# Kernel optimization log

Measured on AMD Instinct MI355X. Metric: run time of the kernel, lower is better.

The kernel has to match this reference:

```python
import jax, jax.numpy as jnp
import numpy as np

N, C, K, NUM_CLASS = 400000, 128, 128, 128


def setup_inputs() -> dict:
    key = jax.random.key(0)
    k1, k2, k3 = jax.random.split(key, 3)
    outputs = jax.random.normal(k1, (N, C), dtype=jnp.float32)
    labels = jax.random.randint(k2, (N,), 0, 2 * NUM_CLASS, dtype=jnp.int64 if jax.config.read('jax_enable_x64') else jnp.int32)
    global_logit = jax.random.normal(k3, (K, C), dtype=jnp.float32)
    return {"outputs": outputs, "labels": labels, "global_logit": global_logit, "k": NUM_CLASS}


def _pairwise_dist(x, protos):
    # Euclidean distance ||proto_j - x_i|| for all (i, j) without a [N,K,C] temp.
    x2 = jnp.sum(x * x, axis=1, keepdims=True)            # [N,1]
    p2 = jnp.sum(protos * protos, axis=1)[None, :]        # [1,K]
    d2 = x2 + p2 - 2.0 * (x @ protos.T)                   # [N,K]
    return jnp.sqrt(jnp.maximum(d2, 0.0))


def reference(outputs, labels, global_logit, k):
    # Rows with labels <= k-1 keep their label; rows with labels > k-1 get the
    # nearest-prototype index. Since the concatenated (labeled + pseudo-labeled)
    # set covers every row and CE-mean is order-invariant, we compute per-row
    # effective labels and a single mean cross-entropy.
    dists = _pairwise_dist(outputs, global_logit)          # [N,K]
    min_dist_labels = jnp.argmin(dists, axis=1)            # [N]
    is_labeled = labels <= (k - 1)
    labels_eff = jnp.where(is_labeled, labels, min_dist_labels)
    logp = jax.nn.log_softmax(outputs, axis=-1)            # [N,C]
    nll = -jnp.take_along_axis(logp, labels_eff[:, None].astype(jnp.int32), axis=1)[:, 0]
    return jnp.mean(nll)
```

## Files before the change

kernel.cpp:

```cpp
#include <hip/hip_runtime.h>
#include <hip/hip_bf16.h>


#define C_DIM 128
#define TILE_ROWS 32
#define NTHREADS 256
#define XSTRIDE 136
#define GRID 2048

typedef __bf16 bf16x8 __attribute__((ext_vector_type(8)));
typedef unsigned short ushort8 __attribute__((ext_vector_type(8)));
typedef float f32x4 __attribute__((ext_vector_type(4)));

union FragU { ushort8 u; bf16x8 b; };

__device__ __forceinline__ unsigned short f2bf(float f) {
    unsigned int u = __float_as_uint(f);
    u += 0x7fffu + ((u >> 16) & 1u);
    return (unsigned short)(u >> 16);
}
__device__ __forceinline__ float bf2f(unsigned short h) {
    return __uint_as_float(((unsigned int)h) << 16);
}
__device__ __forceinline__ unsigned f2ord(float s) {
    unsigned u = __float_as_uint(s);
    return (u & 0x80000000u) ? ~u : (u | 0x80000000u);
}

extern "C" __global__ void __launch_bounds__(NTHREADS)
ploss_main(const float* __restrict__ x, const int* __restrict__ labels,
           const float* __restrict__ protos, const int* __restrict__ kptr,
           float* __restrict__ accum, int n_tiles)
{
    __shared__ __attribute__((aligned(16))) unsigned short x_lds[2][TILE_ROWS * XSTRIDE];
    __shared__ float lse_lds[2][TILE_ROWS];
    __shared__ unsigned wmin_u[4][TILE_ROWS];

    const int tid  = threadIdx.x;
    const int lane = tid & 63;
    const int wave = tid >> 6;
    const int l15  = lane & 15;
    const int quad = lane >> 4;
    const int kk   = kptr[0];

    FragU bfrag[2][4];
    float p2h[2];
#pragma unroll
    for (int nt = 0; nt < 2; ++nt) {
        const int j = wave * 32 + nt * 16 + l15;
        const float* pr = protos + j * C_DIM;
        float s = 0.f;
#pragma unroll
        for (int c = 0; c < 32; c += 4) {
            float4 v = *(const float4*)(pr + quad * 32 + c);
            s += v.x*v.x + v.y*v.y + v.z*v.z + v.w*v.w;
        }
        s += __shfl_xor(s, 16);
        s += __shfl_xor(s, 32);
        p2h[nt] = 0.5f * s;
#pragma unroll
        for (int kt = 0; kt < 4; ++kt) {
            const float* pp = pr + kt * 32 + quad * 8;
            float4 v0 = *(const float4*)(pp);
            float4 v1 = *(const float4*)(pp + 4);
            FragU f;
            f.u[0]=f2bf(v0.x); f.u[1]=f2bf(v0.y); f.u[2]=f2bf(v0.z); f.u[3]=f2bf(v0.w);
            f.u[4]=f2bf(v1.x); f.u[5]=f2bf(v1.y); f.u[6]=f2bf(v1.z); f.u[7]=f2bf(v1.w);
            bfrag[nt][kt] = f;
        }
    }

    const int row_r = tid >> 3;
    const int row_q = tid & 7;

    float nll_acc = 0.f;
    int p = 0;

    int t = blockIdx.x;
    float4 a0, a1, a2, a3;
    int lab = 0;
    {
        const float* xr = x + ((long long)t * TILE_ROWS + row_r) * C_DIM + row_q * 16;
        a0 = *(const float4*)(xr);
        a1 = *(const float4*)(xr + 4);
        a2 = *(const float4*)(xr + 8);
        a3 = *(const float4*)(xr + 12);
        if (tid < TILE_ROWS) lab = labels[(long long)t * TILE_ROWS + tid];
    }

    for (; t < n_tiles; t += GRID) {
        const int tn = t + GRID;
        const int tl = (tn < n_tiles) ? tn : t;
        float4 b0, b1, b2, b3;
        int labn = 0;
        {
            const float* xr = x + ((long long)tl * TILE_ROWS + row_r) * C_DIM + row_q * 16;
            b0 = *(const float4*)(xr);
            b1 = *(const float4*)(xr + 4);
            b2 = *(const float4*)(xr + 8);
            b3 = *(const float4*)(xr + 12);
            if (tid < TILE_ROWS) labn = labels[(long long)tl * TILE_ROWS + tid];
        }

        float m = fmaxf(fmaxf(fmaxf(a0.x,a0.y),fmaxf(a0.z,a0.w)),
                        fmaxf(fmaxf(a1.x,a1.y),fmaxf(a1.z,a1.w)));
        m = fmaxf(m, fmaxf(fmaxf(fmaxf(a2.x,a2.y),fmaxf(a2.z,a2.w)),
                           fmaxf(fmaxf(a3.x,a3.y),fmaxf(a3.z,a3.w))));
        float s = __expf(a0.x-m)+__expf(a0.y-m)+__expf(a0.z-m)+__expf(a0.w-m)
                + __expf(a1.x-m)+__expf(a1.y-m)+__expf(a1.z-m)+__expf(a1.w-m)
                + __expf(a2.x-m)+__expf(a2.y-m)+__expf(a2.z-m)+__expf(a2.w-m)
                + __expf(a3.x-m)+__expf(a3.y-m)+__expf(a3.z-m)+__expf(a3.w-m);
#pragma unroll
        for (int mask = 1; mask <= 4; mask <<= 1) {
            float mo = __shfl_xor(m, mask);
            float so = __shfl_xor(s, mask);
            float nm = fmaxf(m, mo);
            s = s * __expf(m - nm) + so * __expf(mo - nm);
            m = nm;
        }
        if (row_q == 0) lse_lds[p][row_r] = m + __logf(s);

        FragU w0, w1;
        w0.u[0]=f2bf(a0.x); w0.u[1]=f2bf(a0.y); w0.u[2]=f2bf(a0.z); w0.u[3]=f2bf(a0.w);
        w0.u[4]=f2bf(a1.x); w0.u[5]=f2bf(a1.y); w0.u[6]=f2bf(a1.z); w0.u[7]=f2bf(a1.w);
        w1.u[0]=f2bf(a2.x); w1.u[1]=f2bf(a2.y); w1.u[2]=f2bf(a2.z); w1.u[3]=f2bf(a2.w);
        w1.u[4]=f2bf(a3.x); w1.u[5]=f2bf(a3.y); w1.u[6]=f2bf(a3.z); w1.u[7]=f2bf(a3.w);
        ushort8* dst = (ushort8*)&x_lds[p][row_r * XSTRIDE + row_q * 16];
        dst[0] = w0.u;
        dst[1] = w1.u;

        __syncthreads();

        f32x4 acc[2][2];
        f32x4 zero = {0.f, 0.f, 0.f, 0.f};
        acc[0][0]=zero; acc[0][1]=zero; acc[1][0]=zero; acc[1][1]=zero;
#pragma unroll
        for (int kt = 0; kt < 4; ++kt) {
#pragma unroll
            for (int mt = 0; mt < 2; ++mt) {
                FragU af;
                af.u = *(const ushort8*)&x_lds[p][(mt*16 + l15) * XSTRIDE + kt*32 + quad*8];
                acc[mt][0] = __builtin_amdgcn_mfma_f32_16x16x32_bf16(af.b, bfrag[0][kt].b, acc[mt][0], 0, 0, 0);
                acc[mt][1] = __builtin_amdgcn_mfma_f32_16x16x32_bf16(af.b, bfrag[1][kt].b, acc[mt][1], 0, 0, 0);
            }
        }

        const unsigned j0 = (unsigned)(wave*32 + l15);
#pragma unroll
        for (int mt = 0; mt < 2; ++mt) {
#pragma unroll
            for (int reg = 0; reg < 4; ++reg) {
                unsigned u0 = (f2ord(p2h[0] - acc[mt][0][reg]) & 0xFFFFFF80u) | j0;
                unsigned u1 = (f2ord(p2h[1] - acc[mt][1][reg]) & 0xFFFFFF80u) | (j0 + 16u);
                unsigned u = u0 < u1 ? u0 : u1;
#pragma unroll
                for (int mask = 1; mask <= 8; mask <<= 1) {
                    unsigned uo = __shfl_xor(u, mask);
                    u = uo < u ? uo : u;
                }
                if (l15 == 0) wmin_u[wave][mt*16 + quad*4 + reg] = u;
            }
        }
        __syncthreads();

        if (tid < TILE_ROWS) {
            unsigned u = wmin_u[0][tid];
            unsigned u1 = wmin_u[1][tid]; u = u1 < u ? u1 : u;
            unsigned u2 = wmin_u[2][tid]; u = u2 < u ? u2 : u;
            unsigned u3 = wmin_u[3][tid]; u = u3 < u ? u3 : u;
            const int bj = (int)(u & 127u);
            const int eff = (lab <= kk - 1) ? lab : bj;
            const float xv = bf2f(x_lds[p][tid * XSTRIDE + eff]);
            nll_acc += lse_lds[p][tid] - xv;
        }

        a0 = b0; a1 = b1; a2 = b2; a3 = b3; lab = labn;
        p ^= 1;
    }

    if (wave == 0) {
        float v = nll_acc;
#pragma unroll
        for (int mask = 32; mask >= 1; mask >>= 1) v += __shfl_xor(v, mask);
        if (lane == 0) atomicAdd(accum, v);
    }
}

extern "C" __global__ void ploss_finalize(const float* __restrict__ accum,
                                          float* __restrict__ out, float inv_n)
{
    out[0] = accum[0] * inv_n;
}

extern "C" void kernel_launch(void* const* d_in, const int* in_sizes, int n_in,
                              void* d_out, int out_size, void* d_ws, size_t ws_size,
                              hipStream_t stream)
{
    const float* x      = (const float*)d_in[0];
    const int*   labels = (const int*)d_in[1];
    const float* protos = (const float*)d_in[2];
    const int*   kptr   = (const int*)d_in[3];
    const int n_rows  = in_sizes[0] / C_DIM;
    const int n_tiles = n_rows / TILE_ROWS;

    float* accum = (float*)d_ws;
    hipMemsetAsync(accum, 0, sizeof(float), stream);

    int grid = GRID;
    if (grid > n_tiles) grid = n_tiles;
    ploss_main<<<grid, NTHREADS, 0, stream>>>(x, labels, protos, kptr, accum, n_tiles);
    ploss_finalize<<<1, 1, 0, stream>>>(accum, (float*)d_out, 1.0f / (float)n_rows);
}
```

Before: 310.7 us.

## Restructure loss kernel to per-wave 16-row tiles with LDS-staged prototypes

Reorganises the kernel so each wave owns 16 rows of a 64-row tile and computes all 128 prototype columns itself. Prototype bf16 fragments are staged once in LDS instead of held in registers, and the cross-wave argmin reduction plus both per-tile __syncthreads are removed. The global atomic is replaced by per-block partials summed in a double-precision finalize kernel, and the grid is reduced to 1536 blocks with a launch-bounds occupancy hint. In exchange, every MFMA step now reads B fragments from LDS, and more x data is held in registers per thread.

```diff
diff --git a/kernel.cpp b/kernel.cpp
--- a/kernel.cpp
+++ b/kernel.cpp
@@ -1,12 +1,12 @@
 #include <hip/hip_runtime.h>
-#include <hip/hip_bf16.h>
 
 
 #define C_DIM 128
-#define TILE_ROWS 32
+#define TILE_ROWS 64
 #define NTHREADS 256
 #define XSTRIDE 136
-#define GRID 2048
+#define GRID_MAX 1536
+#define NFRAG 32
 
 typedef __bf16 bf16x8 __attribute__((ext_vector_type(8)));
 typedef unsigned short ushort8 __attribute__((ext_vector_type(8)));
@@ -26,170 +26,212 @@
     unsigned u = __float_as_uint(s);
     return (u & 0x80000000u) ? ~u : (u | 0x80000000u);
 }
-
-extern "C" __global__ void __launch_bounds__(NTHREADS)
+__device__ __forceinline__ float fmax4(float4 v) {
+    return fmaxf(fmaxf(v.x, v.y), fmaxf(v.z, v.w));
+}
+__device__ __forceinline__ float esum4(float4 v, float m) {
+    return __expf(v.x - m) + __expf(v.y - m) + __expf(v.z - m) + __expf(v.w - m);
+}
+
+extern "C" __global__ void __launch_bounds__(NTHREADS, 3)
 ploss_main(const float* __restrict__ x, const int* __restrict__ labels,
            const float* __restrict__ protos, const int* __restrict__ kptr,
-           float* __restrict__ accum, int n_tiles)
+           float* __restrict__ partial, int n_tiles, int n_rows)
 {
-    __shared__ __attribute__((aligned(16))) unsigned short x_lds[2][TILE_ROWS * XSTRIDE];
-    __shared__ float lse_lds[2][TILE_ROWS];
-    __shared__ unsigned wmin_u[4][TILE_ROWS];
+    __shared__ __attribute__((aligned(16))) unsigned short blds[NFRAG * 64 * 8];
+    __shared__ __attribute__((aligned(16))) unsigned short x_lds[TILE_ROWS * XSTRIDE];
+    __shared__ float lse_lds[TILE_ROWS];
+    __shared__ float norm_lds[C_DIM];
+    __shared__ float wsum[4];
 
     const int tid  = threadIdx.x;
     const int lane = tid & 63;
     const int wave = tid >> 6;
     const int l15  = lane & 15;
     const int quad = lane >> 4;
-    const int kk   = kptr[0];
-
-    FragU bfrag[2][4];
-    float p2h[2];
-#pragma unroll
-    for (int nt = 0; nt < 2; ++nt) {
-        const int j = wave * 32 + nt * 16 + l15;
-        const float* pr = protos + j * C_DIM;
+    const int r_l  = lane >> 2;
+    const int c_l  = (lane & 3) * 32;
+    const int wrow = wave * 16;
+    const bool epi = (l15 == 0);
+    const int kk = kptr[0];
+
+    {
+        const int j = tid >> 1;
+        const float* pr = protos + j * C_DIM + (tid & 1) * 64;
         float s = 0.f;
 #pragma unroll
-        for (int c = 0; c < 32; c += 4) {
-            float4 v = *(const float4*)(pr + quad * 32 + c);
+        for (int c = 0; c < 64; c += 4) {
+            float4 v = *(const float4*)(pr + c);
             s += v.x*v.x + v.y*v.y + v.z*v.z + v.w*v.w;
         }
-        s += __shfl_xor(s, 16);
-        s += __shfl_xor(s, 32);
-        p2h[nt] = 0.5f * s;
-#pragma unroll
-        for (int kt = 0; kt < 4; ++kt) {
-            const float* pp = pr + kt * 32 + quad * 8;
-            float4 v0 = *(const float4*)(pp);
-            float4 v1 = *(const float4*)(pp + 4);
-            FragU f;
-            f.u[0]=f2bf(v0.x); f.u[1]=f2bf(v0.y); f.u[2]=f2bf(v0.z); f.u[3]=f2bf(v0.w);
-            f.u[4]=f2bf(v1.x); f.u[5]=f2bf(v1.y); f.u[6]=f2bf(v1.z); f.u[7]=f2bf(v1.w);
-            bfrag[nt][kt] = f;
-        }
-    }
-
-    const int row_r = tid >> 3;
-    const int row_q = tid & 7;
+        s += __shfl_xor(s, 1);
+        if ((tid & 1) == 0) norm_lds[j] = s;
+    }
+#pragma unroll
+    for (int f = 0; f < 8; ++f) {
+        const int g = f * NTHREADS + tid;
+        const int l = g & 63;
+        const int frag = g >> 6;
+        const int nt = frag >> 2, kt = frag & 3;
+        const float* pp = protos + (nt * 16 + (l & 15)) * C_DIM + kt * 32 + (l >> 4) * 8;
+        float4 v0 = *(const float4*)(pp);
+        float4 v1 = *(const float4*)(pp + 4);
+        FragU fr;
+        fr.u[0]=f2bf(v0.x); fr.u[1]=f2bf(v0.y); fr.u[2]=f2bf(v0.z); fr.u[3]=f2bf(v0.w);
+        fr.u[4]=f2bf(v1.x); fr.u[5]=f2bf(v1.y); fr.u[6]=f2bf(v1.z); fr.u[7]=f2bf(v1.w);
+        *(ushort8*)&blds[g * 8] = fr.u;
+    }
+    __syncthreads();
+
+    float p2h[8];
+#pragma unroll
+    for (int nt = 0; nt < 8; ++nt) p2h[nt] = 0.5f * norm_lds[nt * 16 + l15];
 
     float nll_acc = 0.f;
-    int p = 0;
 
     int t = blockIdx.x;
-    float4 a0, a1, a2, a3;
-    int lab = 0;
+    float4 a[8];
+    int4 lab4 = {0, 0, 0, 0};
     {
-        const float* xr = x + ((long long)t * TILE_ROWS + row_r) * C_DIM + row_q * 16;
-        a0 = *(const float4*)(xr);
-        a1 = *(const float4*)(xr + 4);
-        a2 = *(const float4*)(xr + 8);
-        a3 = *(const float4*)(xr + 12);
-        if (tid < TILE_ROWS) lab = labels[(long long)t * TILE_ROWS + tid];
-    }
-
-    for (; t < n_tiles; t += GRID) {
-        const int tn = t + GRID;
+        long long rb = (long long)t * TILE_ROWS + wrow + r_l;
+        if (rb >= n_rows) rb = n_rows - 1;
+        const float* xr = x + rb * C_DIM + c_l;
+#pragma unroll
+        for (int i = 0; i < 8; ++i) a[i] = *(const float4*)(xr + i * 4);
+        if (epi) {
+            long long lb = (long long)t * TILE_ROWS + wrow + quad * 4;
+            if (lb > (long long)n_rows - 4) lb = n_rows - 4;
+            lab4 = *(const int4*)(labels + lb);
+        }
+    }
+
+    for (; t < n_tiles; t += gridDim.x) {
+        const int tn = t + gridDim.x;
         const int tl = (tn < n_tiles) ? tn : t;
-        float4 b0, b1, b2, b3;
-        int labn = 0;
+        float4 b[8];
+        int4 labn4 = lab4;
         {
-            const float* xr = x + ((long long)tl * TILE_ROWS + row_r) * C_DIM + row_q * 16;
-            b0 = *(const float4*)(xr);
-            b1 = *(const float4*)(xr + 4);
-            b2 = *(const float4*)(xr + 8);
-            b3 = *(const float4*)(xr + 12);
-            if (tid < TILE_ROWS) labn = labels[(long long)tl * TILE_ROWS + tid];
-        }
-
-        float m = fmaxf(fmaxf(fmaxf(a0.x,a0.y),fmaxf(a0.z,a0.w)),
-                        fmaxf(fmaxf(a1.x,a1.y),fmaxf(a1.z,a1.w)));
-        m = fmaxf(m, fmaxf(fmaxf(fmaxf(a2.x,a2.y),fmaxf(a2.z,a2.w)),
-                           fmaxf(fmaxf(a3.x,a3.y),fmaxf(a3.z,a3.w))));
-        float s = __expf(a0.x-m)+__expf(a0.y-m)+__expf(a0.z-m)+__expf(a0.w-m)
-                + __expf(a1.x-m)+__expf(a1.y-m)+__expf(a1.z-m)+__expf(a1.w-m)
-                + __expf(a2.x-m)+__expf(a2.y-m)+__expf(a2.z-m)+__expf(a2.w-m)
-                + __expf(a3.x-m)+__expf(a3.y-m)+__expf(a3.z-m)+__expf(a3.w-m);
-#pragma unroll
-        for (int mask = 1; mask <= 4; mask <<= 1) {
+            long long rb = (long long)tl * TILE_ROWS + wrow + r_l;
+            if (rb >= n_rows) rb = n_rows - 1;
+            const float* xr = x + rb * C_DIM + c_l;
+#pragma unroll
+            for (int i = 0; i < 8; ++i) b[i] = *(const float4*)(xr + i * 4);
+            if (epi) {
+                long long lb = (long long)tl * TILE_ROWS + wrow + quad * 4;
+                if (lb > (long long)n_rows - 4) lb = n_rows - 4;
+                labn4 = *(const int4*)(labels + lb);
+            }
+        }
+
+        float m = fmax4(a[0]);
+#pragma unroll
+        for (int i = 1; i < 8; ++i) m = fmaxf(m, fmax4(a[i]));
+        float s = 0.f;
+#pragma unroll
+        for (int i = 0; i < 8; ++i) s += esum4(a[i], m);
+#pragma unroll
+        for (int mask = 1; mask <= 2; mask <<= 1) {
             float mo = __shfl_xor(m, mask);
             float so = __shfl_xor(s, mask);
             float nm = fmaxf(m, mo);
             s = s * __expf(m - nm) + so * __expf(mo - nm);
             m = nm;
         }
-        if (row_q == 0) lse_lds[p][row_r] = m + __logf(s);
-
-        FragU w0, w1;
-        w0.u[0]=f2bf(a0.x); w0.u[1]=f2bf(a0.y); w0.u[2]=f2bf(a0.z); w0.u[3]=f2bf(a0.w);
-        w0.u[4]=f2bf(a1.x); w0.u[5]=f2bf(a1.y); w0.u[6]=f2bf(a1.z); w0.u[7]=f2bf(a1.w);
-        w1.u[0]=f2bf(a2.x); w1.u[1]=f2bf(a2.y); w1.u[2]=f2bf(a2.z); w1.u[3]=f2bf(a2.w);
-        w1.u[4]=f2bf(a3.x); w1.u[5]=f2bf(a3.y); w1.u[6]=f2bf(a3.z); w1.u[7]=f2bf(a3.w);
-        ushort8* dst = (ushort8*)&x_lds[p][row_r * XSTRIDE + row_q * 16];
-        dst[0] = w0.u;
-        dst[1] = w1.u;
-
-        __syncthreads();
-
-        f32x4 acc[2][2];
+        if ((lane & 3) == 0) lse_lds[wrow + r_l] = m + __logf(s);
+
+        ushort8* dst = (ushort8*)&x_lds[(wrow + r_l) * XSTRIDE + c_l];
+#pragma unroll
+        for (int i = 0; i < 4; ++i) {
+            float4 v0 = a[2 * i], v1 = a[2 * i + 1];
+            FragU wv;
+            wv.u[0]=f2bf(v0.x); wv.u[1]=f2bf(v0.y); wv.u[2]=f2bf(v0.z); wv.u[3]=f2bf(v0.w);
+            wv.u[4]=f2bf(v1.x); wv.u[5]=f2bf(v1.y); wv.u[6]=f2bf(v1.z); wv.u[7]=f2bf(v1.w);
+            dst[i] = wv.u;
+        }
+        asm volatile("s_waitcnt lgkmcnt(0)" ::: "memory");
+        __builtin_amdgcn_sched_barrier(0);
+
+        FragU A[4];
+#pragma unroll
+        for (int kt = 0; kt < 4; ++kt)
+            A[kt].u = *(const ushort8*)&x_lds[(wrow + l15) * XSTRIDE + kt * 32 + quad * 8];
+        f32x4 acc[8];
         f32x4 zero = {0.f, 0.f, 0.f, 0.f};
-        acc[0][0]=zero; acc[0][1]=zero; acc[1][0]=zero; acc[1][1]=zero;
+#pragma unroll
+        for (int nt = 0; nt < 8; ++nt) acc[nt] = zero;
 #pragma unroll
         for (int kt = 0; kt < 4; ++kt) {
 #pragma unroll
-            for (int mt = 0; mt < 2; ++mt) {
-                FragU af;
-                af.u = *(const ushort8*)&x_lds[p][(mt*16 + l15) * XSTRIDE + kt*32 + quad*8];
-                acc[mt][0] = __builtin_amdgcn_mfma_f32_16x16x32_bf16(af.b, bfrag[0][kt].b, acc[mt][0], 0, 0, 0);
-                acc[mt][1] = __builtin_amdgcn_mfma_f32_16x16x32_bf16(af.b, bfrag[1][kt].b, acc[mt][1], 0, 0, 0);
-            }
-        }
-
-        const unsigned j0 = (unsigned)(wave*32 + l15);
-#pragma unroll
-        for (int mt = 0; mt < 2; ++mt) {
-#pragma unroll
-            for (int reg = 0; reg < 4; ++reg) {
-                unsigned u0 = (f2ord(p2h[0] - acc[mt][0][reg]) & 0xFFFFFF80u) | j0;
-                unsigned u1 = (f2ord(p2h[1] - acc[mt][1][reg]) & 0xFFFFFF80u) | (j0 + 16u);
-                unsigned u = u0 < u1 ? u0 : u1;
-#pragma unroll
-                for (int mask = 1; mask <= 8; mask <<= 1) {
-                    unsigned uo = __shfl_xor(u, mask);
-                    u = uo < u ? uo : u;
+            for (int nt = 0; nt < 8; ++nt) {
+                FragU B;
+                B.u = *(const ushort8*)&blds[((nt * 4 + kt) * 64 + lane) * 8];
+                acc[nt] = __builtin_amdgcn_mfma_f32_16x16x32_bf16(A[kt].b, B.b, acc[nt], 0, 0, 0);
+            }
+        }
+
+        unsigned res[4];
+#pragma unroll
+        for (int rg = 0; rg < 4; ++rg) {
+            unsigned u = 0xFFFFFFFFu;
+#pragma unroll
+            for (int nt = 0; nt < 8; ++nt) {
+                unsigned c = (f2ord(p2h[nt] - acc[nt][rg]) & 0xFFFFFF80u)
+                           | (unsigned)(nt * 16 + l15);
+                u = (c < u) ? c : u;
+            }
+#pragma unroll
+            for (int mask = 1; mask <= 8; mask <<= 1) {
+                unsigned uo = __shfl_xor(u, mask);
+                u = (uo < u) ? uo : u;
+            }
+            res[rg] = u;
+        }
+
+        if (epi) {
+#pragma unroll
+            for (int rg = 0; rg < 4; ++rg) {
+                const int row16 = quad * 4 + rg;
+                const long long grow = (long long)t * TILE_ROWS + wrow + row16;
+                if (grow < n_rows) {
+                    int lab;
+                    if      (rg == 0) lab = lab4.x;
+                    else if (rg == 1) lab = lab4.y;
+                    else if (rg == 2) lab = lab4.z;
+                    else              lab = lab4.w;
+                    const int bj  = (int)(res[rg] & 127u);
+                    const int eff = (lab <= kk - 1) ? lab : bj;
+                    const float xv = bf2f(x_lds[(wrow + row16) * XSTRIDE + eff]);
+                    nll_acc += lse_lds[wrow + row16] - xv;
                 }
-                if (l15 == 0) wmin_u[wave][mt*16 + quad*4 + reg] = u;
-            }
-        }
-        __syncthreads();
-
-        if (tid < TILE_ROWS) {
-            unsigned u = wmin_u[0][tid];
-            unsigned u1 = wmin_u[1][tid]; u = u1 < u ? u1 : u;
-            unsigned u2 = wmin_u[2][tid]; u = u2 < u ? u2 : u;
-            unsigned u3 = wmin_u[3][tid]; u = u3 < u ? u3 : u;
-            const int bj = (int)(u & 127u);
-            const int eff = (lab <= kk - 1) ? lab : bj;
-            const float xv = bf2f(x_lds[p][tid * XSTRIDE + eff]);
-            nll_acc += lse_lds[p][tid] - xv;
-        }
-
-        a0 = b0; a1 = b1; a2 = b2; a3 = b3; lab = labn;
-        p ^= 1;
-    }
-
-    if (wave == 0) {
-        float v = nll_acc;
-#pragma unroll
-        for (int mask = 32; mask >= 1; mask >>= 1) v += __shfl_xor(v, mask);
-        if (lane == 0) atomicAdd(accum, v);
-    }
-}
-
-extern "C" __global__ void ploss_finalize(const float* __restrict__ accum,
-                                          float* __restrict__ out, float inv_n)
+            }
+        }
+
+#pragma unroll
+        for (int i = 0; i < 8; ++i) a[i] = b[i];
+        lab4 = labn4;
+    }
+
+    float v = nll_acc;
+#pragma unroll
+    for (int mask = 1; mask <= 32; mask <<= 1) v += __shfl_xor(v, mask);
+    if (lane == 0) wsum[wave] = v;
+    __syncthreads();
+    if (tid == 0) partial[blockIdx.x] = wsum[0] + wsum[1] + wsum[2] + wsum[3];
+}
+
+extern "C" __global__ void __launch_bounds__(256)
+ploss_finalize(const float* __restrict__ partial, float* __restrict__ out,
+               float inv_n, int nparts)
 {
-    out[0] = accum[0] * inv_n;
+    __shared__ double sm[4];
+    const int tid = threadIdx.x, lane = tid & 63, wave = tid >> 6;
+    double v = 0.0;
+    for (int i = tid; i < nparts; i += 256) v += (double)partial[i];
+#pragma unroll
+    for (int mask = 1; mask <= 32; mask <<= 1) v += __shfl_xor(v, mask);
+    if (lane == 0) sm[wave] = v;
+    __syncthreads();
+    if (tid == 0) out[0] = (float)((sm[0] + sm[1] + sm[2] + sm[3]) * (double)inv_n);
 }
 
 extern "C" void kernel_launch(void* const* d_in, const int* in_sizes, int n_in,
@@ -201,13 +243,18 @@
     const float* protos = (const float*)d_in[2];
     const int*   kptr   = (const int*)d_in[3];
     const int n_rows  = in_sizes[0] / C_DIM;
-    const int n_tiles = n_rows / TILE_ROWS;
-
-    float* accum = (float*)d_ws;
-    hipMemsetAsync(accum, 0, sizeof(float), stream);
-
-    int grid = GRID;
+    const int n_tiles = (n_rows + TILE_ROWS - 1) / TILE_ROWS;
+
+    float* partial = (float*)d_ws;
+
+    int grid = GRID_MAX;
     if (grid > n_tiles) grid = n_tiles;
-    ploss_main<<<grid, NTHREADS, 0, stream>>>(x, labels, protos, kptr, accum, n_tiles);
-    ploss_finalize<<<1, 1, 0, stream>>>(accum, (float*)d_out, 1.0f / (float)n_rows);
-}
+    const int max_parts = (int)(ws_size / sizeof(float));
+    if (grid > max_parts) grid = max_parts;
+    if (grid < 1) grid = 1;
+
+    ploss_main<<<grid, NTHREADS, 0, stream>>>(x, labels, protos, kptr, partial,
+                                              n_tiles, n_rows);
+    ploss_finalize<<<1, 256, 0, stream>>>(partial, (float*)d_out,
+                                          1.0f / (float)n_rows, grid);
+}
```

Measured after the change: 298.3 us. -4.0%, faster.
